# Kernel optimization log

Hardware: AMD Instinct MI355X
Metric: run time of the kernel (lower is better)

Reference implementation:

```python
import jax, jax.numpy as jnp
import numpy as np

# ---- model dims (match init_kwargs) ----
HIDDEN = 2048
N_HEADS = 16
Q_LORA = 768
KV_LORA = 512
NOPE = 128
ROPE = 64
V_DIM = 128
QK_HEAD = NOPE + ROPE  # 192
EPS = 1e-6


def _rms_norm(x, w):
    var = jnp.mean(jnp.square(x), axis=-1, keepdims=True)
    return x * jax.lax.rsqrt(var + EPS) * w


def _rotate_half(x):
    x1, x2 = jnp.split(x, 2, axis=-1)
    return jnp.concatenate([-x2, x1], axis=-1)


def _apply_rotary(x, cos, sin):
    # x: (b, h, s, d_r); cos/sin: (b, s, d_r) -> broadcast over heads
    c = cos[:, None, :, :]
    s = sin[:, None, :, :]
    return x * c + _rotate_half(x) * s


def setup_inputs() -> dict:
    key = jax.random.key(0)
    ks = jax.random.split(key, 8)
    B, S = 2, 2048

    hidden_states = jax.random.normal(ks[0], (B, S, HIDDEN), dtype=jnp.float32)

    # proper rotary cos/sin tables on the decoupled rope sub-dimension
    inv_freq = 1.0 / (10000.0 ** (np.arange(0, ROPE, 2, dtype=np.float32) / ROPE))
    pos = np.arange(S, dtype=np.float32)
    ang = np.einsum('s,d->sd', pos, inv_freq)           # (S, ROPE/2)
    emb = np.concatenate([ang, ang], axis=-1)           # (S, ROPE)
    cos = jnp.broadcast_to(jnp.asarray(np.cos(emb)), (B, S, ROPE)).astype(jnp.float32)
    sin = jnp.broadcast_to(jnp.asarray(np.sin(emb)), (B, S, ROPE)).astype(jnp.float32)

    # causal additive mask (1,1,S,S)
    neg = jnp.finfo(jnp.float32).min
    causal = jnp.where(jnp.tril(jnp.ones((S, S), dtype=bool)), 0.0, neg)
    attention_mask = causal[None, None, :, :]

    sd = 0.02
    wq_a = jax.random.normal(ks[1], (Q_LORA, HIDDEN), dtype=jnp.float32) * sd
    q_norm_w = jnp.ones((Q_LORA,), dtype=jnp.float32)
    wq_b = jax.random.normal(ks[2], (N_HEADS * QK_HEAD, Q_LORA), dtype=jnp.float32) * sd
    wkv_a = jax.random.normal(ks[3], (KV_LORA + ROPE, HIDDEN), dtype=jnp.float32) * sd
    kv_norm_w = jnp.ones((KV_LORA,), dtype=jnp.float32)
    wkv_b = jax.random.normal(ks[4], (N_HEADS * (NOPE + V_DIM), KV_LORA), dtype=jnp.float32) * sd
    wo = jax.random.normal(ks[5], (HIDDEN, N_HEADS * V_DIM), dtype=jnp.float32) * sd

    return dict(hidden_states=hidden_states, cos=cos, sin=sin,
                attention_mask=attention_mask, wq_a=wq_a, q_norm_w=q_norm_w,
                wq_b=wq_b, wkv_a=wkv_a, kv_norm_w=kv_norm_w, wkv_b=wkv_b, wo=wo)


def reference(hidden_states, cos, sin, attention_mask,
              wq_a, q_norm_w, wq_b, wkv_a, kv_norm_w, wkv_b, wo):
    B, S, _ = hidden_states.shape
    scaling = QK_HEAD ** -0.5

    # low-rank query projection: down -> RMSNorm -> up
    q = _rms_norm(hidden_states @ wq_a.T, q_norm_w) @ wq_b.T   # (B,S,H*QK_HEAD)
    q = q.reshape(B, S, N_HEADS, QK_HEAD).transpose(0, 2, 1, 3)  # (B,H,S,QK_HEAD)
    q_nope, q_pe = q[..., :NOPE], q[..., NOPE:]
    q_pe = _apply_rotary(q_pe, cos, sin)                        # (B,H,S,ROPE)

    # low-rank kv projection: latent + decoupled rope key
    kv_full = hidden_states @ wkv_a.T                           # (B,S,KV_LORA+ROPE)
    kv_lat, k_pe = kv_full[..., :KV_LORA], kv_full[..., KV_LORA:]
    k_pe = _apply_rotary(k_pe[:, None, :, :], cos, sin)         # (B,1,S,ROPE)

    # matrix absorption: fold wkv_b's k-part into q_nope
    wkv_b_h = wkv_b.reshape(N_HEADS, NOPE + V_DIM, KV_LORA)     # (H, NOPE+V, C)
    q_lat = jnp.einsum('bhsd,hdc->bhsc', q_nope, wkv_b_h[:, :NOPE])  # (B,H,S,C)

    kv = _rms_norm(kv_lat, kv_norm_w)[:, None, :, :]            # (B,1,S,C)

    # attention scores against the latent cache + rope key
    attn = (jnp.einsum('bhsc,bktc->bhst', q_lat, kv) +
            jnp.einsum('bhsr,bktr->bhst', q_pe, k_pe)) * scaling  # (B,H,S,S)
    attn = attn + attention_mask[:, :, :, :S]
    attn_weights = jax.nn.softmax(attn.astype(jnp.float32), axis=-1).astype(q_lat.dtype)

    # aggregate latent values, then absorb wkv_b's v-part
    ctx = jnp.einsum('bhst,bktc->bhsc', attn_weights, kv)       # (B,H,S,C)
    out = jnp.einsum('bhsc,hdc->bhsd', ctx, wkv_b_h[:, NOPE:])  # (B,H,S,V)
    out = out.transpose(0, 2, 1, 3).reshape(B, S, N_HEADS * V_DIM)
    attn_output = out @ wo.T                                    # (B,S,HIDDEN)
    return attn_output, attn_weights
```

## Files before the change

kernel.cpp:

```cpp
#include <hip/hip_runtime.h>
#include <stdint.h>

#define S_LEN   2048
#define B_SZ    2
#define HIDDEN  2048
#define N_HEADS 16
#define Q_LORA  768
#define KV_LORA 512
#define NOPE    128
#define ROPE    64
#define V_DIM   128
#define QK_HEAD 192
#define KEXT    576
#define EPSV    1e-6f

#define TRI_Z   2228224

typedef __attribute__((ext_vector_type(8))) short bf16x8;
typedef __attribute__((ext_vector_type(4))) float f32x4;

__device__ __forceinline__ unsigned short f2bf(float f){
  union { float f; unsigned u; } v; v.f = f;
  unsigned u = v.u;
  return (unsigned short)((u + 0x7FFFu + ((u >> 16) & 1u)) >> 16);
}
__device__ __forceinline__ float bf2f(unsigned short h){
  union { unsigned u; float f; } v; v.u = ((unsigned)h) << 16; return v.f;
}

__device__ __forceinline__ void gload16(const unsigned short* g, unsigned short* l){
  __builtin_amdgcn_global_load_lds((const __attribute__((address_space(1))) void*)g,
                                   (__attribute__((address_space(3))) void*)l, 16, 0, 0);
}

__global__ void cast_f32_bf16(const float* __restrict__ in, unsigned short* __restrict__ out, int n4){
  int i = blockIdx.x * blockDim.x + threadIdx.x;
  if (i >= n4) return;
  float4 v = ((const float4*)in)[i];
  ushort4 o;
  o.x = f2bf(v.x); o.y = f2bf(v.y); o.z = f2bf(v.z); o.w = f2bf(v.w);
  ((ushort4*)out)[i] = o;
}

__global__ void transpose_tile(const unsigned short* __restrict__ in, unsigned short* __restrict__ out,
                               int ldin, long inStride, int ldout, long outStride){
  __shared__ unsigned short t[64][65];
  int r0 = blockIdx.y * 64, c0 = blockIdx.x * 64;
  const unsigned short* ib = in + (long)blockIdx.z * inStride;
  unsigned short* ob = out + (long)blockIdx.z * outStride;
  int tid = threadIdx.x;
  #pragma unroll
  for (int i = 0; i < 16; i++) {
    int idx = i * 256 + tid;
    int lr = idx >> 6, lc = idx & 63;
    t[lr][lc] = ib[(long)(r0 + lr) * ldin + c0 + lc];
  }
  __syncthreads();
  #pragma unroll
  for (int i = 0; i < 16; i++) {
    int idx = i * 256 + tid;
    int lr = idx >> 6, lc = idx & 63;
    ob[(long)(c0 + lr) * ldout + r0 + lc] = t[lc][lr];
  }
}

template<bool C_F32, bool TRI_A, bool SKIP_UPPER>
__launch_bounds__(256)
__global__ void gemm_kernel(const unsigned short* __restrict__ A, const unsigned short* __restrict__ B,
                            void* __restrict__ Cv,
                            int M, int N, int K, int lda, int ldb, int ldc,
                            long strideA, long strideB,
                            int bdiv, int bmod,
                            int cdiv, long cstride1, int cmod, long cstride2,
                            float alpha)
{
  if (SKIP_UPPER && blockIdx.x > blockIdx.y) return;

  __shared__ __align__(16) unsigned short As[128*32];
  __shared__ __align__(16) unsigned short Bs[128*32];

  int z  = blockIdx.z;
  int m0 = blockIdx.y * 128;
  int n0 = blockIdx.x * 128;
  int idxB = (z / bdiv) % bmod;
  const unsigned short* Bb = B + (long)idxB * strideB;
  long cOff = (long)(z / cdiv) * cstride1 + (long)(z % cmod) * cstride2;

  int kmax = TRI_A ? (m0 + 128) : K;
  long aBase;
  if (TRI_A) {
    int rt = m0 >> 7;
    aBase = (long)z * strideA + (long)(rt * (rt + 1) / 2) * 16384;
  } else {
    aBase = (long)z * strideA;
  }

  int tid  = threadIdx.x;
  int lane = tid & 63;
  int wid  = tid >> 6;
  int wm   = (wid & 1) * 64;
  int wn   = (wid >> 1) * 64;
  int lrow = lane & 15;
  int kgrp = lane >> 4;

  int sR = wid * 16 + (lane >> 2);
  int sC = (lane & 3) * 8;
  int aStr = TRI_A ? kmax : lda;
  const unsigned short* aP = A + aBase + (TRI_A ? 0L : (long)m0 * lda) + (long)sR * aStr + sC;
  const unsigned short* bP = Bb + (long)(n0 + sR) * ldb + sC;
  unsigned short* ldsA = &As[wid * 512];
  unsigned short* ldsB = &Bs[wid * 512];

  f32x4 zero = {0.f, 0.f, 0.f, 0.f};
  f32x4 acc[4][4];
  #pragma unroll
  for (int i = 0; i < 4; i++)
    #pragma unroll
    for (int j = 0; j < 4; j++) acc[i][j] = zero;

  for (int k0 = 0; k0 < kmax; k0 += 32) {
    gload16(aP + k0,                      ldsA);
    gload16(aP + (long)64 * aStr + k0,    ldsA + 2048);
    gload16(bP + k0,                      ldsB);
    gload16(bP + (long)64 * ldb + k0,     ldsB + 2048);
    __syncthreads();

    bf16x8 af[4], bfg[4];
    #pragma unroll
    for (int mt = 0; mt < 4; mt++)
      af[mt] = *(const bf16x8*)&As[(wm + mt*16 + lrow)*32 + kgrp*8];
    #pragma unroll
    for (int nt = 0; nt < 4; nt++)
      bfg[nt] = *(const bf16x8*)&Bs[(wn + nt*16 + lrow)*32 + kgrp*8];
    #pragma unroll
    for (int mt = 0; mt < 4; mt++)
      #pragma unroll
      for (int nt = 0; nt < 4; nt++)
        acc[mt][nt] = __builtin_amdgcn_mfma_f32_16x16x32_bf16(af[mt], bfg[nt], acc[mt][nt], 0, 0, 0);
    __syncthreads();
  }

  #pragma unroll
  for (int mt = 0; mt < 4; mt++) {
    #pragma unroll
    for (int nt = 0; nt < 4; nt++) {
      int col = n0 + wn + nt*16 + lrow;
      if (col >= N) continue;
      int rowb = m0 + wm + mt*16 + kgrp*4;
      #pragma unroll
      for (int r = 0; r < 4; r++) {
        int row = rowb + r;
        if (row >= M) continue;
        float v = acc[mt][nt][r] * alpha;
        if (C_F32) ((float*)Cv)[cOff + (long)row * ldc + col] = v;
        else ((unsigned short*)Cv)[cOff + (long)row * ldc + col] = f2bf(v);
      }
    }
  }
}

__global__ void rmsnorm_q(const float* __restrict__ in, const float* __restrict__ w,
                          unsigned short* __restrict__ out){
  __shared__ float red[4];
  int row = blockIdx.x;
  const float* x = in + (size_t)row * Q_LORA;
  int tid = threadIdx.x;
  float v0 = x[tid], v1 = x[tid + 256], v2 = x[tid + 512];
  float s = v0*v0 + v1*v1 + v2*v2;
  #pragma unroll
  for (int o = 32; o > 0; o >>= 1) s += __shfl_xor(s, o, 64);
  int lane = tid & 63, wid = tid >> 6;
  if (lane == 0) red[wid] = s;
  __syncthreads();
  float tot = red[0] + red[1] + red[2] + red[3];
  float r = rsqrtf(tot * (1.0f / Q_LORA) + EPSV);
  unsigned short* op = out + (size_t)row * Q_LORA;
  op[tid]       = f2bf(v0 * r * w[tid]);
  op[tid + 256] = f2bf(v1 * r * w[tid + 256]);
  op[tid + 512] = f2bf(v2 * r * w[tid + 512]);
}

__global__ void kv_prep(const float* __restrict__ kvf, const float* __restrict__ w,
                        const float* __restrict__ cosb, const float* __restrict__ sinb,
                        unsigned short* __restrict__ kext){
  __shared__ float red[4];
  int row = blockIdx.x;
  const float* x = kvf + (size_t)row * KEXT;
  int tid = threadIdx.x;
  float v0 = x[tid], v1 = x[tid + 256];
  float s = v0*v0 + v1*v1;
  #pragma unroll
  for (int o = 32; o > 0; o >>= 1) s += __shfl_xor(s, o, 64);
  int lane = tid & 63, wid = tid >> 6;
  if (lane == 0) red[wid] = s;
  __syncthreads();
  float tot = red[0] + red[1] + red[2] + red[3];
  float r = rsqrtf(tot * (1.0f / KV_LORA) + EPSV);
  unsigned short* op = kext + (size_t)row * KEXT;
  op[tid]       = f2bf(v0 * r * w[tid]);
  op[tid + 256] = f2bf(v1 * r * w[tid + 256]);
  if (tid < 64) {
    int i = tid;
    float xi = x[512 + i];
    float other = (i < 32) ? -x[512 + i + 32] : x[512 + i - 32];
    float c  = cosb[(size_t)row * 64 + i];
    float sn = sinb[(size_t)row * 64 + i];
    op[512 + i] = f2bf(xi * c + other * sn);
  }
}

__global__ void q_prep(const unsigned short* __restrict__ qfull, const float* __restrict__ cosb,
                       const float* __restrict__ sinb, unsigned short* __restrict__ qnope,
                       unsigned short* __restrict__ qext){
  int row = blockIdx.x;
  int h   = blockIdx.y;
  int b   = row >> 11;
  int s_  = row & 2047;
  const unsigned short* x = qfull + (size_t)row * (N_HEADS * QK_HEAD) + h * QK_HEAD;
  int tid = threadIdx.x;
  long base = ((long)(b * N_HEADS + h) * S_LEN + s_);
  if (tid < 128) {
    qnope[base * NOPE + tid] = x[tid];
  } else {
    int i = tid - 128;
    float xi = bf2f(x[128 + i]);
    float other = (i < 32) ? -bf2f(x[128 + i + 32]) : bf2f(x[128 + i - 32]);
    float c  = cosb[(size_t)row * 64 + i];
    float sn = sinb[(size_t)row * 64 + i];
    qext[base * KEXT + 512 + i] = f2bf(xi * c + other * sn);
  }
}

__global__ void softmax_rows(float* __restrict__ scores, unsigned short* __restrict__ probs){
  __shared__ float red[4];
  int gid = blockIdx.x;
  int z = gid >> 11;
  int r = gid & 2047;
  float* x = scores + (size_t)gid * S_LEN;
  int rt = r >> 7;
  int rowlen = (rt + 1) << 7;
  unsigned short* prow = probs + (long)z * TRI_Z + (long)(rt * (rt + 1) / 2) * 16384
                         + (long)(r - (rt << 7)) * rowlen;
  int tid = threadIdx.x;
  float v[8];
  #pragma unroll
  for (int i = 0; i < 8; i++) {
    int idx = tid + i * 256;
    v[i] = (idx <= r) ? x[idx] : -3.4028234663852886e38f;
  }
  float m = v[0];
  #pragma unroll
  for (int i = 1; i < 8; i++) m = fmaxf(m, v[i]);
  #pragma unroll
  for (int o = 32; o > 0; o >>= 1) m = fmaxf(m, __shfl_xor(m, o, 64));
  int lane = tid & 63, wid = tid >> 6;
  if (lane == 0) red[wid] = m;
  __syncthreads();
  m = fmaxf(fmaxf(red[0], red[1]), fmaxf(red[2], red[3]));
  __syncthreads();
  float s = 0.f;
  #pragma unroll
  for (int i = 0; i < 8; i++) {
    int idx = tid + i * 256;
    v[i] = (idx <= r) ? __expf(v[i] - m) : 0.f;
    s += v[i];
  }
  #pragma unroll
  for (int o = 32; o > 0; o >>= 1) s += __shfl_xor(s, o, 64);
  if (lane == 0) red[wid] = s;
  __syncthreads();
  s = red[0] + red[1] + red[2] + red[3];
  float inv = 1.0f / s;
  #pragma unroll
  for (int i = 0; i < 8; i++) {
    int idx = tid + i * 256;
    float p = v[i] * inv;
    x[idx] = p;
    if (idx < rowlen) prow[idx] = f2bf(p);
  }
}

extern "C" void kernel_launch(void* const* d_in, const int* in_sizes, int n_in,
                              void* d_out, int out_size, void* d_ws, size_t ws_size,
                              hipStream_t stream) {
  const float* hs    = (const float*)d_in[0];
  const float* cosb  = (const float*)d_in[1];
  const float* sinb  = (const float*)d_in[2];
  const float* wq_a  = (const float*)d_in[4];
  const float* q_nw  = (const float*)d_in[5];
  const float* wq_b  = (const float*)d_in[6];
  const float* wkv_a = (const float*)d_in[7];
  const float* kv_nw = (const float*)d_in[8];
  const float* wkv_b = (const float*)d_in[9];
  const float* wo    = (const float*)d_in[10];

  float* attn_out = (float*)d_out;
  float* scores   = attn_out + (size_t)B_SZ * S_LEN * HIDDEN;

  char* ws = (char*)d_ws;
  const size_t o_wkvb  = 0;
  const size_t o_wo    = 4194304;
  const size_t AR      = 16777216;
  const size_t o_wqa   = AR + 0;
  const size_t o_wqb   = AR + 3145728;
  const size_t o_wkva  = AR + 7864320;
  const size_t o_wkvbT = AR + 10223616;
  const size_t o_hs    = AR + 12320768;
  const size_t o_qa    = AR + 29097984;
  const size_t o_qn    = AR + 41680896;
  const size_t o_qfull = AR + 47972352;
  const size_t o_kvf   = AR + 73138176;
  const size_t o_kext  = AR + 82575360;
  const size_t o_qnope = AR + 87293952;
  const size_t o_qext  = AR + 104071168;
  const size_t o_probs = AR + 0;
  const size_t o_vwT   = AR + 142606336;
  const size_t o_outc  = AR + 176160768;
  const size_t total   = AR + 192937984;
  if (ws_size < total) return;

  unsigned short* wkvb_bf = (unsigned short*)(ws + o_wkvb);
  unsigned short* wo_bf   = (unsigned short*)(ws + o_wo);
  unsigned short* wqa_bf  = (unsigned short*)(ws + o_wqa);
  unsigned short* wqb_bf  = (unsigned short*)(ws + o_wqb);
  unsigned short* wkva_bf = (unsigned short*)(ws + o_wkva);
  unsigned short* wkvbT   = (unsigned short*)(ws + o_wkvbT);
  unsigned short* hs_bf   = (unsigned short*)(ws + o_hs);
  float*          qa      = (float*)(ws + o_qa);
  unsigned short* qn      = (unsigned short*)(ws + o_qn);
  unsigned short* qfull   = (unsigned short*)(ws + o_qfull);
  float*          kvf     = (float*)(ws + o_kvf);
  unsigned short* kext    = (unsigned short*)(ws + o_kext);
  unsigned short* qnope   = (unsigned short*)(ws + o_qnope);
  unsigned short* qext    = (unsigned short*)(ws + o_qext);
  unsigned short* probs   = (unsigned short*)(ws + o_probs);
  unsigned short* vwT     = (unsigned short*)(ws + o_vwT);
  unsigned short* outcat  = (unsigned short*)(ws + o_outc);

  auto cast = [&](const float* src, unsigned short* dst, size_t n){
    int n4 = (int)(n / 4);
    cast_f32_bf16<<<dim3((n4 + 255) / 256), dim3(256), 0, stream>>>(src, dst, n4);
  };
  cast(hs,    hs_bf,   (size_t)4096*2048);
  cast(wq_a,  wqa_bf,  (size_t)768*2048);
  cast(wq_b,  wqb_bf,  (size_t)3072*768);
  cast(wkv_a, wkva_bf, (size_t)576*2048);
  cast(wkv_b, wkvb_bf, (size_t)4096*512);
  cast(wo,    wo_bf,   (size_t)2048*2048);

  transpose_tile<<<dim3(8,2,16),256,0,stream>>>(wkvb_bf, wkvbT, 512, 131072L, 128, 65536L);

  gemm_kernel<true,false,false><<<dim3(6,32,1),256,0,stream>>>(
      hs_bf, wqa_bf, qa, 4096, 768, 2048, 2048, 2048, 768,
      0L, 0L, 1, 1, 1, 0L, 1, 0L, 1.0f);
  rmsnorm_q<<<dim3(4096),dim3(256),0,stream>>>(qa, q_nw, qn);
  gemm_kernel<false,false,false><<<dim3(24,32,1),256,0,stream>>>(
      qn, wqb_bf, qfull, 4096, 3072, 768, 768, 768, 3072,
      0L, 0L, 1, 1, 1, 0L, 1, 0L, 1.0f);
  gemm_kernel<true,false,false><<<dim3(5,32,1),256,0,stream>>>(
      hs_bf, wkva_bf, kvf, 4096, 576, 2048, 2048, 2048, 576,
      0L, 0L, 1, 1, 1, 0L, 1, 0L, 1.0f);
  kv_prep<<<dim3(4096),dim3(256),0,stream>>>(kvf, kv_nw, cosb, sinb, kext);
  q_prep<<<dim3(4096,16),dim3(192),0,stream>>>(qfull, cosb, sinb, qnope, qext);
  gemm_kernel<false,false,false><<<dim3(4,16,32),256,0,stream>>>(
      qnope, wkvbT, qext, 2048, 512, 128, 128, 128, 576,
      262144L, 65536L, 1, 16, 1, 1179648L, 1, 0L, 1.0f);
  gemm_kernel<true,false,true><<<dim3(16,16,32),256,0,stream>>>(
      qext, kext, scores, 2048, 2048, 576, 576, 576, 2048,
      1179648L, 1179648L, 16, 1000000, 1, 4194304L, 1, 0L,
      0.07216878364870322f);
  for (int b = 0; b < B_SZ; b++) {
    gemm_kernel<false,false,false><<<dim3(16,1,16),256,0,stream>>>(
        wkvb_bf + 65536, kext + (long)b * 2048 * KEXT, vwT + (long)b * 4194304,
        128, 2048, 512, 512, KEXT, 2048,
        131072L, 0L, 1, 1, 1, 262144L, 1, 0L, 1.0f);
  }
  softmax_rows<<<dim3(65536),dim3(256),0,stream>>>(scores, probs);
  for (int b = 0; b < B_SZ; b++) {
    gemm_kernel<false,true,false><<<dim3(1,16,16),256,0,stream>>>(
        probs + (long)b * 16 * TRI_Z, vwT + (long)b * 4194304, outcat + (long)b * 4194304,
        2048, 128, 2048, 0, 2048, 2048,
        (long)TRI_Z, 262144L, 1, 16, 1, 0L, 16, 128L, 1.0f);
  }
  gemm_kernel<true,false,false><<<dim3(16,32,1),256,0,stream>>>(
      outcat, wo_bf, attn_out, 4096, 2048, 2048, 2048, 2048, 2048,
      0L, 0L, 1, 1, 1, 0L, 1, 0L, 1.0f);
}
```

Measured before the change: 1.374 ms.

## Fuse casts and q/kv down-projections, batch per-batch GEMMs, deepen GEMM K-step

Replaces six cast launches with one combined cast kernel. Places wq_a and wkv_a next to each other so a single GEMM produces both down-projections into one buffer with row stride 1344. Folds the per-batch loops for the V-weight GEMM and the PV GEMM into single launches by adding separate A-index div/mod parameters. Doubles the GEMM K-step to 64 by staging two 32-wide slices per barrier, which halves the synchronisations but doubles LDS use per block.

```diff
diff --git a/kernel.cpp b/kernel.cpp
--- a/kernel.cpp
+++ b/kernel.cpp
@@ -13,6 +13,7 @@
 #define QK_HEAD 192
 #define KEXT    576
 #define EPSV    1e-6f
+#define QKC_LD  1344
 
 #define TRI_Z   2228224
 
@@ -33,13 +34,31 @@
                                    (__attribute__((address_space(3))) void*)l, 16, 0, 0);
 }
 
-__global__ void cast_f32_bf16(const float* __restrict__ in, unsigned short* __restrict__ out, int n4){
+#define C_HS   2097152
+#define C_WQA  (C_HS   + 393216)
+#define C_WQB  (C_WQA  + 589824)
+#define C_WKVA (C_WQB  + 294912)
+#define C_WKVB (C_WKVA + 524288)
+#define C_WO   (C_WKVB + 1048576)
+__global__ void cast_all(const float* __restrict__ hs, const float* __restrict__ wqa,
+                         const float* __restrict__ wqb, const float* __restrict__ wkva,
+                         const float* __restrict__ wkvb, const float* __restrict__ wo,
+                         unsigned short* __restrict__ d_hs, unsigned short* __restrict__ d_wqa,
+                         unsigned short* __restrict__ d_wqb, unsigned short* __restrict__ d_wkva,
+                         unsigned short* __restrict__ d_wkvb, unsigned short* __restrict__ d_wo){
   int i = blockIdx.x * blockDim.x + threadIdx.x;
-  if (i >= n4) return;
-  float4 v = ((const float4*)in)[i];
+  const float* s; unsigned short* d; int j;
+  if      (i < C_HS)   { s = hs;   d = d_hs;   j = i; }
+  else if (i < C_WQA)  { s = wqa;  d = d_wqa;  j = i - C_HS; }
+  else if (i < C_WQB)  { s = wqb;  d = d_wqb;  j = i - C_WQA; }
+  else if (i < C_WKVA) { s = wkva; d = d_wkva; j = i - C_WQB; }
+  else if (i < C_WKVB) { s = wkvb; d = d_wkvb; j = i - C_WKVA; }
+  else if (i < C_WO)   { s = wo;   d = d_wo;   j = i - C_WKVB; }
+  else return;
+  float4 v = ((const float4*)s)[j];
   ushort4 o;
   o.x = f2bf(v.x); o.y = f2bf(v.y); o.z = f2bf(v.z); o.w = f2bf(v.w);
-  ((ushort4*)out)[i] = o;
+  ((ushort4*)d)[j] = o;
 }
 
 __global__ void transpose_tile(const unsigned short* __restrict__ in, unsigned short* __restrict__ out,
@@ -70,18 +89,20 @@
                             void* __restrict__ Cv,
                             int M, int N, int K, int lda, int ldb, int ldc,
                             long strideA, long strideB,
+                            int adiv, int amod,
                             int bdiv, int bmod,
                             int cdiv, long cstride1, int cmod, long cstride2,
                             float alpha)
 {
   if (SKIP_UPPER && blockIdx.x > blockIdx.y) return;
 
-  __shared__ __align__(16) unsigned short As[128*32];
-  __shared__ __align__(16) unsigned short Bs[128*32];
+  __shared__ __align__(16) unsigned short As[2*128*32];
+  __shared__ __align__(16) unsigned short Bs[2*128*32];
 
   int z  = blockIdx.z;
   int m0 = blockIdx.y * 128;
   int n0 = blockIdx.x * 128;
+  int idxA = (z / adiv) % amod;
   int idxB = (z / bdiv) % bmod;
   const unsigned short* Bb = B + (long)idxB * strideB;
   long cOff = (long)(z / cdiv) * cstride1 + (long)(z % cmod) * cstride2;
@@ -90,9 +111,9 @@
   long aBase;
   if (TRI_A) {
     int rt = m0 >> 7;
-    aBase = (long)z * strideA + (long)(rt * (rt + 1) / 2) * 16384;
+    aBase = (long)idxA * strideA + (long)(rt * (rt + 1) / 2) * 16384;
   } else {
-    aBase = (long)z * strideA;
+    aBase = (long)idxA * strideA;
   }
 
   int tid  = threadIdx.x;
@@ -118,25 +139,32 @@
     #pragma unroll
     for (int j = 0; j < 4; j++) acc[i][j] = zero;
 
-  for (int k0 = 0; k0 < kmax; k0 += 32) {
-    gload16(aP + k0,                      ldsA);
-    gload16(aP + (long)64 * aStr + k0,    ldsA + 2048);
-    gload16(bP + k0,                      ldsB);
-    gload16(bP + (long)64 * ldb + k0,     ldsB + 2048);
+  for (int k0 = 0; k0 < kmax; k0 += 64) {
+    gload16(aP + k0,                             ldsA);
+    gload16(aP + (long)64 * aStr + k0,           ldsA + 2048);
+    gload16(aP + (k0 + 32),                      ldsA + 4096);
+    gload16(aP + (long)64 * aStr + (k0 + 32),    ldsA + 4096 + 2048);
+    gload16(bP + k0,                             ldsB);
+    gload16(bP + (long)64 * ldb + k0,            ldsB + 2048);
+    gload16(bP + (k0 + 32),                      ldsB + 4096);
+    gload16(bP + (long)64 * ldb + (k0 + 32),     ldsB + 4096 + 2048);
     __syncthreads();
 
-    bf16x8 af[4], bfg[4];
     #pragma unroll
-    for (int mt = 0; mt < 4; mt++)
-      af[mt] = *(const bf16x8*)&As[(wm + mt*16 + lrow)*32 + kgrp*8];
-    #pragma unroll
-    for (int nt = 0; nt < 4; nt++)
-      bfg[nt] = *(const bf16x8*)&Bs[(wn + nt*16 + lrow)*32 + kgrp*8];
-    #pragma unroll
-    for (int mt = 0; mt < 4; mt++)
+    for (int kk = 0; kk < 2; kk++) {
+      bf16x8 af[4], bfg[4];
+      #pragma unroll
+      for (int mt = 0; mt < 4; mt++)
+        af[mt] = *(const bf16x8*)&As[kk*4096 + (wm + mt*16 + lrow)*32 + kgrp*8];
       #pragma unroll
       for (int nt = 0; nt < 4; nt++)
-        acc[mt][nt] = __builtin_amdgcn_mfma_f32_16x16x32_bf16(af[mt], bfg[nt], acc[mt][nt], 0, 0, 0);
+        bfg[nt] = *(const bf16x8*)&Bs[kk*4096 + (wn + nt*16 + lrow)*32 + kgrp*8];
+      #pragma unroll
+      for (int mt = 0; mt < 4; mt++)
+        #pragma unroll
+        for (int nt = 0; nt < 4; nt++)
+          acc[mt][nt] = __builtin_amdgcn_mfma_f32_16x16x32_bf16(af[mt], bfg[nt], acc[mt][nt], 0, 0, 0);
+    }
     __syncthreads();
   }
 
@@ -163,7 +191,7 @@
                           unsigned short* __restrict__ out){
   __shared__ float red[4];
   int row = blockIdx.x;
-  const float* x = in + (size_t)row * Q_LORA;
+  const float* x = in + (size_t)row * QKC_LD;
   int tid = threadIdx.x;
   float v0 = x[tid], v1 = x[tid + 256], v2 = x[tid + 512];
   float s = v0*v0 + v1*v1 + v2*v2;
@@ -180,12 +208,12 @@
   op[tid + 512] = f2bf(v2 * r * w[tid + 512]);
 }
 
-__global__ void kv_prep(const float* __restrict__ kvf, const float* __restrict__ w,
+__global__ void kv_prep(const float* __restrict__ qkc, const float* __restrict__ w,
                         const float* __restrict__ cosb, const float* __restrict__ sinb,
                         unsigned short* __restrict__ kext){
   __shared__ float red[4];
   int row = blockIdx.x;
-  const float* x = kvf + (size_t)row * KEXT;
+  const float* x = qkc + (size_t)row * QKC_LD + Q_LORA;
   int tid = threadIdx.x;
   float v0 = x[tid], v1 = x[tid + 256];
   float s = v0*v0 + v1*v1;
@@ -302,14 +330,13 @@
   const size_t o_wo    = 4194304;
   const size_t AR      = 16777216;
   const size_t o_wqa   = AR + 0;
-  const size_t o_wqb   = AR + 3145728;
-  const size_t o_wkva  = AR + 7864320;
+  const size_t o_wkva  = AR + 3145728;
+  const size_t o_wqb   = AR + 5505024;
   const size_t o_wkvbT = AR + 10223616;
   const size_t o_hs    = AR + 12320768;
-  const size_t o_qa    = AR + 29097984;
-  const size_t o_qn    = AR + 41680896;
-  const size_t o_qfull = AR + 47972352;
-  const size_t o_kvf   = AR + 73138176;
+  const size_t o_qkc   = AR + 29097984;
+  const size_t o_qn    = AR + 51118080;
+  const size_t o_qfull = AR + 57409536;
   const size_t o_kext  = AR + 82575360;
   const size_t o_qnope = AR + 87293952;
   const size_t o_qext  = AR + 104071168;
@@ -322,14 +349,13 @@
   unsigned short* wkvb_bf = (unsigned short*)(ws + o_wkvb);
   unsigned short* wo_bf   = (unsigned short*)(ws + o_wo);
   unsigned short* wqa_bf  = (unsigned short*)(ws + o_wqa);
+  unsigned short* wkva_bf = (unsigned short*)(ws + o_wkva);
   unsigned short* wqb_bf  = (unsigned short*)(ws + o_wqb);
-  unsigned short* wkva_bf = (unsigned short*)(ws + o_wkva);
   unsigned short* wkvbT   = (unsigned short*)(ws + o_wkvbT);
   unsigned short* hs_bf   = (unsigned short*)(ws + o_hs);
-  float*          qa      = (float*)(ws + o_qa);
+  float*          qkc     = (float*)(ws + o_qkc);
   unsigned short* qn      = (unsigned short*)(ws + o_qn);
   unsigned short* qfull   = (unsigned short*)(ws + o_qfull);
-  float*          kvf     = (float*)(ws + o_kvf);
   unsigned short* kext    = (unsigned short*)(ws + o_kext);
   unsigned short* qnope   = (unsigned short*)(ws + o_qnope);
   unsigned short* qext    = (unsigned short*)(ws + o_qext);
@@ -337,52 +363,36 @@
   unsigned short* vwT     = (unsigned short*)(ws + o_vwT);
   unsigned short* outcat  = (unsigned short*)(ws + o_outc);
 
-  auto cast = [&](const float* src, unsigned short* dst, size_t n){
-    int n4 = (int)(n / 4);
-    cast_f32_bf16<<<dim3((n4 + 255) / 256), dim3(256), 0, stream>>>(src, dst, n4);
-  };
-  cast(hs,    hs_bf,   (size_t)4096*2048);
-  cast(wq_a,  wqa_bf,  (size_t)768*2048);
-  cast(wq_b,  wqb_bf,  (size_t)3072*768);
-  cast(wkv_a, wkva_bf, (size_t)576*2048);
-  cast(wkv_b, wkvb_bf, (size_t)4096*512);
-  cast(wo,    wo_bf,   (size_t)2048*2048);
+  cast_all<<<dim3((C_WO + 255) / 256), dim3(256), 0, stream>>>(
+      hs, wq_a, wq_b, wkv_a, wkv_b, wo,
+      hs_bf, wqa_bf, wqb_bf, wkva_bf, wkvb_bf, wo_bf);
 
   transpose_tile<<<dim3(8,2,16),256,0,stream>>>(wkvb_bf, wkvbT, 512, 131072L, 128, 65536L);
 
-  gemm_kernel<true,false,false><<<dim3(6,32,1),256,0,stream>>>(
-      hs_bf, wqa_bf, qa, 4096, 768, 2048, 2048, 2048, 768,
-      0L, 0L, 1, 1, 1, 0L, 1, 0L, 1.0f);
-  rmsnorm_q<<<dim3(4096),dim3(256),0,stream>>>(qa, q_nw, qn);
+  gemm_kernel<true,false,false><<<dim3(11,32,1),256,0,stream>>>(
+      hs_bf, wqa_bf, qkc, 4096, 1344, 2048, 2048, 2048, QKC_LD,
+      0L, 0L, 1, 1, 1, 1, 1, 0L, 1, 0L, 1.0f);
+  rmsnorm_q<<<dim3(4096),dim3(256),0,stream>>>(qkc, q_nw, qn);
+  kv_prep<<<dim3(4096),dim3(256),0,stream>>>(qkc, kv_nw, cosb, sinb, kext);
   gemm_kernel<false,false,false><<<dim3(24,32,1),256,0,stream>>>(
       qn, wqb_bf, qfull, 4096, 3072, 768, 768, 768, 3072,
-      0L, 0L, 1, 1, 1, 0L, 1, 0L, 1.0f);
-  gemm_kernel<true,false,false><<<dim3(5,32,1),256,0,stream>>>(
-      hs_bf, wkva_bf, kvf, 4096, 576, 2048, 2048, 2048, 576,
-      0L, 0L, 1, 1, 1, 0L, 1, 0L, 1.0f);
-  kv_prep<<<dim3(4096),dim3(256),0,stream>>>(kvf, kv_nw, cosb, sinb, kext);
+      0L, 0L, 1, 1, 1, 1, 1, 0L, 1, 0L, 1.0f);
   q_prep<<<dim3(4096,16),dim3(192),0,stream>>>(qfull, cosb, sinb, qnope, qext);
   gemm_kernel<false,false,false><<<dim3(4,16,32),256,0,stream>>>(
       qnope, wkvbT, qext, 2048, 512, 128, 128, 128, 576,
-      262144L, 65536L, 1, 16, 1, 1179648L, 1, 0L, 1.0f);
+      262144L, 65536L, 1, 1000000, 1, 16, 1, 1179648L, 1, 0L, 1.0f);
   gemm_kernel<true,false,true><<<dim3(16,16,32),256,0,stream>>>(
       qext, kext, scores, 2048, 2048, 576, 576, 576, 2048,
-      1179648L, 1179648L, 16, 1000000, 1, 4194304L, 1, 0L,
+      1179648L, 1179648L, 1, 1000000, 16, 1000000, 1, 4194304L, 1, 0L,
       0.07216878364870322f);
-  for (int b = 0; b < B_SZ; b++) {
-    gemm_kernel<false,false,false><<<dim3(16,1,16),256,0,stream>>>(
-        wkvb_bf + 65536, kext + (long)b * 2048 * KEXT, vwT + (long)b * 4194304,
-        128, 2048, 512, 512, KEXT, 2048,
-        131072L, 0L, 1, 1, 1, 262144L, 1, 0L, 1.0f);
-  }
+  gemm_kernel<false,false,false><<<dim3(16,1,32),256,0,stream>>>(
+      wkvb_bf + 65536, kext, vwT, 128, 2048, 512, 512, KEXT, 2048,
+      131072L, 1179648L, 1, 16, 16, 2, 1, 262144L, 1, 0L, 1.0f);
   softmax_rows<<<dim3(65536),dim3(256),0,stream>>>(scores, probs);
-  for (int b = 0; b < B_SZ; b++) {
-    gemm_kernel<false,true,false><<<dim3(1,16,16),256,0,stream>>>(
-        probs + (long)b * 16 * TRI_Z, vwT + (long)b * 4194304, outcat + (long)b * 4194304,
-        2048, 128, 2048, 0, 2048, 2048,
-        (long)TRI_Z, 262144L, 1, 16, 1, 0L, 16, 128L, 1.0f);
-  }
+  gemm_kernel<false,true,false><<<dim3(1,16,32),256,0,stream>>>(
+      probs, vwT, outcat, 2048, 128, 2048, 0, 2048, 2048,
+      (long)TRI_Z, 262144L, 1, 1000000, 1, 1000000, 16, 4194304L, 16, 128L, 1.0f);
   gemm_kernel<true,false,false><<<dim3(16,32,1),256,0,stream>>>(
       outcat, wo_bf, attn_out, 4096, 2048, 2048, 2048, 2048, 2048,
-      0L, 0L, 1, 1, 1, 0L, 1, 0L, 1.0f);
-}
+      0L, 0L, 1, 1, 1, 1, 1, 0L, 1, 0L, 1.0f);
+}
```

Measured after the change: 1.212 ms. 1.13x faster.
